# Kernel tuning notes

Measured on AMD Instinct MI355X. Metric: run time of the kernel, lower is better.

Reference implementation:

```python
import jax, jax.numpy as jnp
import numpy as np

FS = 2          # filter_size (kernel == stride, non-overlapping)
NL = 10         # num_layers
C_IN = 3        # input_channels
H = 256         # hidden width
OUT = 10        # out_dim
B = 128         # batch
D = FS ** NL    # input spatial length = 1024


def setup_inputs() -> dict:
    key = jax.random.key(0)
    ks = jax.random.split(key, NL + 2)
    inp = {"x": jax.random.normal(ks[0], (B, C_IN, D), dtype=jnp.float32)}
    cin = C_IN
    for l in range(NL):
        dl = D // FS ** (l + 1)  # out positions at layer l
        inp[f"w{l}"] = jax.random.normal(ks[l + 1], (H, cin, dl, FS), dtype=jnp.float32)
        cin = H
    inp["beta"] = jax.random.normal(ks[-1], (H, OUT), dtype=jnp.float32)
    return inp


def _lc(x, w):
    # Locally-connected 1d, stride == kernel: unfold is a pure reshape.
    # x: (B, C, Dd*k), w: (O, C, Dd, k) -> out: (B, O, Dd)
    O, C, Dd, k = w.shape
    xu = x.reshape(x.shape[0], C, Dd, k)
    # per-position contraction over (C, k); avoids the (B,O,C,Dd,k) intermediate
    return jnp.einsum('bcdk,ocdk->bod', xu, w) / (C ** 0.5)


def reference(x, w0, w1, w2, w3, w4, w5, w6, w7, w8, w9, beta):
    ws = [w0, w1, w2, w3, w4, w5, w6, w7, w8, w9]
    y = x
    for w in ws:  # fixed small layer loop
        y = jax.nn.relu(_lc(y, w))
    y = y.mean(axis=-1)            # (B, H) — last spatial dim is size 1
    return y @ beta / beta.shape[0]  # (B, OUT)
```

## Files before the change

### kernel.cpp

```cpp
#include <hip/hip_runtime.h>
#include <hip/hip_bf16.h>
#include <stdint.h>


typedef __attribute__((ext_vector_type(4))) float floatx4;
typedef __attribute__((ext_vector_type(8))) short shortx8;

__device__ __forceinline__ float bf2f(unsigned short u){
    union { unsigned int u; float f; } c; c.u = ((unsigned int)u) << 16; return c.f;
}
__device__ __forceinline__ unsigned short f2bf(float f){
    union { float f; unsigned int u; } c; c.f = f;
    unsigned int x = c.u;
    x += 0x7FFFu + ((x >> 16) & 1u);
    return (unsigned short)(x >> 16);
}

__global__ void probe_kernel(const unsigned int* __restrict__ x, int* __restrict__ flag){
    __shared__ int cnt[256];
    int tid = threadIdx.x;
    unsigned short lo = (unsigned short)(x[tid] & 0xFFFFu);
    int e = (lo >> 7) & 0xFF;
    cnt[tid] = (e >= 90 && e <= 143) ? 1 : 0;
    __syncthreads();
    for (int s = 128; s > 0; s >>= 1){
        if (tid < s) cnt[tid] += cnt[tid + s];
        __syncthreads();
    }
    if (tid == 0) *flag = (cnt[0] > 160) ? 1 : 0;
}

__global__ __launch_bounds__(256) void l0_kernel(const int* __restrict__ flag,
        const void* __restrict__ xv, const void* __restrict__ wv,
        unsigned short* __restrict__ A1){
    __shared__ float Xs[128*6];
    const int d = blockIdx.x;
    const int tid = threadIdx.x;
    const bool BF = (*flag != 0);
    for (int i = tid; i < 384; i += 256){
        int b = i / 3, c = i - b*3;
        if (BF){
            unsigned int u = *(const unsigned int*)((const unsigned short*)xv + (b*3+c)*1024 + 2*d);
            Xs[b*6 + c*2]     = bf2f((unsigned short)(u & 0xFFFFu));
            Xs[b*6 + c*2 + 1] = bf2f((unsigned short)(u >> 16));
        } else {
            const float* xf = (const float*)xv + (b*3+c)*1024 + 2*d;
            Xs[b*6 + c*2] = xf[0]; Xs[b*6 + c*2 + 1] = xf[1];
        }
    }
    __syncthreads();
    const int o = tid;
    float wr[6];
    #pragma unroll
    for (int c = 0; c < 3; ++c){
        if (BF){
            unsigned int u = *(const unsigned int*)((const unsigned short*)wv + ((o*3+c)*512 + d)*2);
            wr[c*2]   = bf2f((unsigned short)(u & 0xFFFFu));
            wr[c*2+1] = bf2f((unsigned short)(u >> 16));
        } else {
            const float* wf = (const float*)wv + ((o*3+c)*512 + d)*2;
            wr[c*2] = wf[0]; wr[c*2+1] = wf[1];
        }
    }
    const float s3 = 0.57735026918962576f;
    for (int b = 0; b < 128; ++b){
        float s = 0.f;
        #pragma unroll
        for (int j = 0; j < 6; ++j) s += Xs[b*6 + j] * wr[j];
        A1[d*32768 + b*256 + o] = f2bf(fmaxf(s, 0.f) * s3);
    }
}

template<bool WBF, bool ATOMIC>
__device__ __forceinline__ void layer_main_impl(const unsigned short* __restrict__ Ain,
        const void* __restrict__ wv, void* __restrict__ out, int dl, int ks){
    __shared__ unsigned short At[8*128*16];
    __shared__ unsigned short Wt[4*64*40];
    const int tid  = threadIdx.x;
    const int lane = tid & 63, wv_ = tid >> 6;
    const int g = lane >> 4, mr = lane & 15;
    const int nd = dl >> 2;
    int bi = blockIdx.x;
    const int dg = bi % nd; bi /= nd;
    const int ng = bi & 3;
    const int ksid = bi >> 2;
    const int TS = 16 / ks;
    const int d0 = dg << 2;
    const int o0 = ng << 6;
    const int dme = d0 + wv_;
    const float* wF = (const float*)wv;
    const unsigned short* wB = (const unsigned short*)wv;

    floatx4 acc[8][4];
    #pragma unroll
    for (int m = 0; m < 8; ++m)
        #pragma unroll
        for (int nb = 0; nb < 4; ++nb)
            acc[m][nb] = (floatx4){0.f,0.f,0.f,0.f};

    for (int s = 0; s < TS; ++s){
        const int c0 = (ksid*TS + s) << 4;
        {
            const int b = tid >> 1, h = tid & 1;
            #pragma unroll
            for (int i = 0; i < 8; ++i){
                uint4 v = *(const uint4*)(Ain + (2*d0 + i)*32768 + b*256 + c0 + h*8);
                *(uint4*)(At + (i*128 + b)*16 + h*8) = v;
            }
        }
        #pragma unroll
        for (int rr = 0; rr < 4; ++rr){
            int run = (rr << 8) + tid;
            int oo = run >> 4, cl = run & 15;
            int src = ((((o0 + oo) << 8) + (c0 + cl))*dl + d0)*2;
            unsigned short wtmp[8];
            if (WBF){
                uint4 u = *(const uint4*)(wB + src);
                const unsigned short* pu = (const unsigned short*)&u;
                #pragma unroll
                for (int j = 0; j < 8; ++j) wtmp[j] = pu[j];
            } else {
                float4 a = *(const float4*)(wF + src);
                float4 b4 = *(const float4*)(wF + src + 4);
                wtmp[0]=f2bf(a.x); wtmp[1]=f2bf(a.y); wtmp[2]=f2bf(a.z); wtmp[3]=f2bf(a.w);
                wtmp[4]=f2bf(b4.x); wtmp[5]=f2bf(b4.y); wtmp[6]=f2bf(b4.z); wtmp[7]=f2bf(b4.w);
            }
            #pragma unroll
            for (int j = 0; j < 8; ++j){
                int dd = j >> 1, t = j & 1;
                Wt[(dd*64 + oo)*40 + t*16 + cl] = wtmp[j];
            }
        }
        __syncthreads();
        shortx8 bfr[4];
        #pragma unroll
        for (int nb = 0; nb < 4; ++nb)
            bfr[nb] = *(const shortx8*)(Wt + (wv_*64 + nb*16 + mr)*40 + g*8);
        #pragma unroll
        for (int m = 0; m < 8; ++m){
            shortx8 af = *(const shortx8*)(At + ((wv_*2 + (g>>1))*128 + m*16 + mr)*16 + (g&1)*8);
            #pragma unroll
            for (int nb = 0; nb < 4; ++nb)
                acc[m][nb] = __builtin_amdgcn_mfma_f32_16x16x32_bf16(af, bfr[nb], acc[m][nb], 0,0,0);
        }
        __syncthreads();
    }
    #pragma unroll
    for (int m = 0; m < 8; ++m)
        #pragma unroll
        for (int nb = 0; nb < 4; ++nb)
            #pragma unroll
            for (int r = 0; r < 4; ++r){
                int b = m*16 + g*4 + r;
                int o = o0 + nb*16 + mr;
                if (ATOMIC)
                    unsafeAtomicAdd((float*)out + (dme*128 + b)*256 + o, acc[m][nb][r]);
                else
                    ((unsigned short*)out)[dme*32768 + b*256 + o] =
                        f2bf(fmaxf(acc[m][nb][r], 0.f) * 0.0625f);
            }
}

template<bool ATOMIC>
__global__ __launch_bounds__(256,2) void layer_main_k(const int* __restrict__ flag,
        const unsigned short* __restrict__ Ain, const void* __restrict__ wv,
        void* __restrict__ out, int dl, int ks){
    if (*flag) layer_main_impl<true,  ATOMIC>(Ain, wv, out, dl, ks);
    else       layer_main_impl<false, ATOMIC>(Ain, wv, out, dl, ks);
}

template<bool WBF>
__device__ __forceinline__ void tail_impl(const unsigned short* __restrict__ Ain,
        const void* __restrict__ wv, float* __restrict__ outS, int dl, int ksplit){
    int id = blockIdx.x;
    int d = id % dl; int t2 = id / dl;
    int ob = t2 & 3; int ksid = t2 >> 2;
    const int KSEG = 512 / ksplit;
    const int k0s = ksid * KSEG;
    const int lane = threadIdx.x & 63, wv2 = threadIdx.x >> 6;
    const int mr = lane & 15, kg = lane >> 4;
    const float* wF = (const float*)wv;
    const unsigned short* wB = (const unsigned short*)wv;
    floatx4 acc[2][4];
    #pragma unroll
    for (int mi = 0; mi < 2; ++mi)
        #pragma unroll
        for (int ni = 0; ni < 4; ++ni) acc[mi][ni] = (floatx4){0.f,0.f,0.f,0.f};
    for (int k0 = k0s; k0 < k0s + KSEG; k0 += 32){
        int c0 = (k0 >> 1) + kg*4;
        shortx8 af[2];
        #pragma unroll
        for (int mi = 0; mi < 2; ++mi){
            int b = wv2*32 + mi*16 + mr;
            #pragma unroll
            for (int cc = 0; cc < 4; ++cc){
                af[mi][2*cc]   = (short)Ain[(2*d)*32768   + b*256 + c0 + cc];
                af[mi][2*cc+1] = (short)Ain[(2*d+1)*32768 + b*256 + c0 + cc];
            }
        }
        shortx8 bf_[4];
        #pragma unroll
        for (int ni = 0; ni < 4; ++ni){
            int o = ob*64 + ni*16 + mr;
            int base = ((o*256 + c0)*dl + d)*2;
            #pragma unroll
            for (int cc = 0; cc < 4; ++cc){
                if (WBF){
                    unsigned int u = *(const unsigned int*)(wB + base);
                    bf_[ni][2*cc]   = (short)(u & 0xFFFFu);
                    bf_[ni][2*cc+1] = (short)(u >> 16);
                } else {
                    bf_[ni][2*cc]   = (short)f2bf(wF[base]);
                    bf_[ni][2*cc+1] = (short)f2bf(wF[base+1]);
                }
                base += 2*dl;
            }
        }
        #pragma unroll
        for (int mi = 0; mi < 2; ++mi)
            #pragma unroll
            for (int ni = 0; ni < 4; ++ni)
                acc[mi][ni] = __builtin_amdgcn_mfma_f32_16x16x32_bf16(af[mi], bf_[ni], acc[mi][ni], 0,0,0);
    }
    #pragma unroll
    for (int mi = 0; mi < 2; ++mi)
        #pragma unroll
        for (int ni = 0; ni < 4; ++ni)
            #pragma unroll
            for (int r = 0; r < 4; ++r){
                int b = wv2*32 + mi*16 + kg*4 + r;
                int o = ob*64 + ni*16 + mr;
                unsafeAtomicAdd(outS + (d*128 + b)*256 + o, acc[mi][ni][r]);
            }
}
__global__ __launch_bounds__(256) void tail_k(const int* __restrict__ flag,
        const unsigned short* __restrict__ Ain, const void* __restrict__ wv,
        float* __restrict__ outS, int dl, int ksplit){
    if (*flag) tail_impl<true >(Ain, wv, outS, dl, ksplit);
    else       tail_impl<false>(Ain, wv, outS, dl, ksplit);
}

__global__ __launch_bounds__(256) void fin_kernel(const float* __restrict__ S,
        unsigned short* __restrict__ A, int n){
    int i = (blockIdx.x*256 + threadIdx.x)*4;
    if (i + 3 < n){
        float4 v = *(const float4*)(S + i);
        unsigned short r0 = f2bf(fmaxf(v.x,0.f)*0.0625f);
        unsigned short r1 = f2bf(fmaxf(v.y,0.f)*0.0625f);
        unsigned short r2 = f2bf(fmaxf(v.z,0.f)*0.0625f);
        unsigned short r3 = f2bf(fmaxf(v.w,0.f)*0.0625f);
        unsigned int lo = (unsigned int)r0 | ((unsigned int)r1 << 16);
        unsigned int hi = (unsigned int)r2 | ((unsigned int)r3 << 16);
        uint2 u; u.x = lo; u.y = hi;
        *(uint2*)(A + i) = u;
    }
}

template<bool BF>
__device__ __forceinline__ void epi_impl(const float* __restrict__ S9, const void* __restrict__ beta,
                                         void* __restrict__ out){
    int b = blockIdx.x;
    int lane = threadIdx.x;
    float accv[10];
    #pragma unroll
    for (int o = 0; o < 10; ++o) accv[o] = 0.f;
    for (int h = lane; h < 256; h += 64){
        float y = fmaxf(S9[b*256 + h], 0.f) * 0.0625f;
        #pragma unroll
        for (int o = 0; o < 10; ++o){
            float be = BF ? bf2f(((const unsigned short*)beta)[h*10 + o])
                          : ((const float*)beta)[h*10 + o];
            accv[o] += y * be;
        }
    }
    #pragma unroll
    for (int off = 32; off > 0; off >>= 1){
        #pragma unroll
        for (int o = 0; o < 10; ++o)
            accv[o] += __shfl_down(accv[o], off, 64);
    }
    if (lane == 0){
        #pragma unroll
        for (int o = 0; o < 10; ++o){
            float v = accv[o] * (1.f/256.f);
            if (BF) ((unsigned short*)out)[b*10 + o] = f2bf(v);
            else    ((float*)out)[b*10 + o] = v;
        }
    }
}
__global__ void epi_kernel(const int* __restrict__ flag, const float* __restrict__ S9,
                           const void* __restrict__ beta, void* __restrict__ out){
    if (*flag) epi_impl<true>(S9, beta, out);
    else       epi_impl<false>(S9, beta, out);
}

extern "C" void kernel_launch(void* const* d_in, const int* in_sizes, int n_in,
                              void* d_out, int out_size, void* d_ws, size_t ws_size,
                              hipStream_t stream) {
    (void)in_sizes; (void)n_in; (void)out_size; (void)ws_size;
    char* wsb = (char*)d_ws;
    int* flag = (int*)wsb;
    unsigned short* A1 = (unsigned short*)(wsb + 512);
    float* S2 = (float*)(wsb + 512);
    float* S3 = S2 + 4194304;
    float* S4 = S3 + 2097152;
    float* S5 = S4 + 1048576;
    float* S6 = S5 + 524288;
    float* S7 = S6 + 262144;
    float* S8 = S7 + 131072;
    float* S9 = S8 + 65536;
    unsigned short* A2 = (unsigned short*)(wsb + 512 + 33554432);
    unsigned short* A3 = A2;
    unsigned short* A4 = A3 + 4194304;
    unsigned short* A5 = A4 + 2097152;
    unsigned short* A6 = A5 + 1048576;
    unsigned short* A7 = A6 + 524288;
    unsigned short* A8 = A7 + 262144;
    unsigned short* A9 = A8 + 131072;

    probe_kernel<<<1, 256, 0, stream>>>((const unsigned int*)d_in[0], flag);
    l0_kernel<<<512, 256, 0, stream>>>(flag, d_in[0], d_in[1], A1);
    layer_main_k<false><<<256, 256, 0, stream>>>(flag, A1, d_in[2], A2, 256, 1);
    hipMemsetAsync(S2, 0, 33423360, stream);
    layer_main_k<true ><<<256, 256, 0, stream>>>(flag, A2, d_in[3], S2, 128, 2);
    fin_kernel<<<4096, 256, 0, stream>>>(S2, A3, 4194304);
    layer_main_k<true ><<<256, 256, 0, stream>>>(flag, A3, d_in[4], S3, 64, 4);
    fin_kernel<<<2048, 256, 0, stream>>>(S3, A4, 2097152);
    layer_main_k<true ><<<256, 256, 0, stream>>>(flag, A4, d_in[5], S4, 32, 8);
    fin_kernel<<<1024, 256, 0, stream>>>(S4, A5, 1048576);
    layer_main_k<true ><<<256, 256, 0, stream>>>(flag, A5, d_in[6], S5, 16, 16);
    fin_kernel<<<512, 256, 0, stream>>>(S5, A6, 524288);
    layer_main_k<true ><<<128, 256, 0, stream>>>(flag, A6, d_in[7], S6, 8, 16);
    fin_kernel<<<256, 256, 0, stream>>>(S6, A7, 262144);
    layer_main_k<true ><<<64, 256, 0, stream>>>(flag, A7, d_in[8], S7, 4, 16);
    fin_kernel<<<128, 256, 0, stream>>>(S7, A8, 131072);
    tail_k<<<128, 256, 0, stream>>>(flag, A8, d_in[9], S8, 2, 16);
    fin_kernel<<<64, 256, 0, stream>>>(S8, A9, 65536);
    tail_k<<<64, 256, 0, stream>>>(flag, A9, d_in[10], S9, 1, 16);
    epi_kernel<<<128, 64, 0, stream>>>(flag, S9, d_in[11], d_out);
}
```

Baseline: 642.4 us.

## Retile locally-connected layers with batch/output blocking and direct-global A fragments

Replaces the layer_main kernel with layer3_k, which tiles over 32 batch rows × 32 output channels × several positions per wave. A fragments now load straight from global memory instead of staging through LDS, and the weight-tile LDS layout is rearranged and padded. Layer 2 now writes bf16 directly without split-K atomics, which removes its fin pass. The deeper layers get new split-K and grid choices that give more blocks per launch, and workspace offsets are reshuffled. This trades LDS reuse of activations for more parallelism and fewer atomics, at the cost of more global loads per MFMA.

```diff
diff --git a/kernel.cpp b/kernel.cpp
--- a/kernel.cpp
+++ b/kernel.cpp
@@ -3,8 +3,15 @@
 #include <stdint.h>
 
 
+#define B_   128
+#define H_   256
+#define OUT_ 10
+#define WT_PLANE 644
+#define WT_ELEMS (32*WT_PLANE)
+
 typedef __attribute__((ext_vector_type(4))) float floatx4;
 typedef __attribute__((ext_vector_type(8))) short shortx8;
+typedef __attribute__((ext_vector_type(4))) short shortx4;
 
 __device__ __forceinline__ float bf2f(unsigned short u){
     union { unsigned int u; float f; } c; c.u = ((unsigned int)u) << 16; return c.f;
@@ -71,102 +78,124 @@
     }
 }
 
-template<bool WBF, bool ATOMIC>
-__device__ __forceinline__ void layer_main_impl(const unsigned short* __restrict__ Ain,
-        const void* __restrict__ wv, void* __restrict__ out, int dl, int ks){
-    __shared__ unsigned short At[8*128*16];
-    __shared__ unsigned short Wt[4*64*40];
-    const int tid  = threadIdx.x;
+template<int DPW, bool WBF, bool ATOMIC>
+__device__ __forceinline__ void layer3_impl(unsigned short* __restrict__ Wt,
+        const unsigned short* __restrict__ Ain, const void* __restrict__ wv,
+        void* __restrict__ out, int dl, int dgN, int TS){
+    constexpr int DT = 4*DPW;
+    const int tid = threadIdx.x;
     const int lane = tid & 63, wv_ = tid >> 6;
-    const int g = lane >> 4, mr = lane & 15;
-    const int nd = dl >> 2;
+    const int mr = lane & 15, g = lane >> 4;
+    const int tI = g >> 1, chI = g & 1;
     int bi = blockIdx.x;
-    const int dg = bi % nd; bi /= nd;
-    const int ng = bi & 3;
-    const int ksid = bi >> 2;
-    const int TS = 16 / ks;
-    const int d0 = dg << 2;
-    const int o0 = ng << 6;
-    const int dme = d0 + wv_;
+    const int bg = bi & 3; const int og = (bi >> 2) & 7; const int rest = bi >> 5;
+    const int dg = rest % dgN; const int ksid = rest / dgN;
+    const int d0 = dg * DT, o0 = og * 32, b0 = bg * 32;
     const float* wF = (const float*)wv;
     const unsigned short* wB = (const unsigned short*)wv;
 
-    floatx4 acc[8][4];
-    #pragma unroll
-    for (int m = 0; m < 8; ++m)
-        #pragma unroll
-        for (int nb = 0; nb < 4; ++nb)
-            acc[m][nb] = (floatx4){0.f,0.f,0.f,0.f};
+    floatx4 acc[2][2][DPW];
+    #pragma unroll
+    for (int m = 0; m < 2; ++m)
+        #pragma unroll
+        for (int nb = 0; nb < 2; ++nb)
+            #pragma unroll
+            for (int dd = 0; dd < DPW; ++dd)
+                acc[m][nb][dd] = (floatx4){0.f,0.f,0.f,0.f};
 
     for (int s = 0; s < TS; ++s){
         const int c0 = (ksid*TS + s) << 4;
-        {
-            const int b = tid >> 1, h = tid & 1;
-            #pragma unroll
-            for (int i = 0; i < 8; ++i){
-                uint4 v = *(const uint4*)(Ain + (2*d0 + i)*32768 + b*256 + c0 + h*8);
-                *(uint4*)(At + (i*128 + b)*16 + h*8) = v;
-            }
-        }
-        #pragma unroll
-        for (int rr = 0; rr < 4; ++rr){
-            int run = (rr << 8) + tid;
-            int oo = run >> 4, cl = run & 15;
-            int src = ((((o0 + oo) << 8) + (c0 + cl))*dl + d0)*2;
-            unsigned short wtmp[8];
-            if (WBF){
-                uint4 u = *(const uint4*)(wB + src);
-                const unsigned short* pu = (const unsigned short*)&u;
+        if (WBF){
+            constexpr int PARTS = DT/4;
+            for (int task = tid; task < 512*PARTS; task += 256){
+                int part = (PARTS == 1) ? 0 : (task & (PARTS-1));
+                int run  = (PARTS == 1) ? task : (task / PARTS);
+                int cl = run & 15, ol = run >> 4;
+                const unsigned short* src = wB + ((size_t)((o0+ol)*256 + c0+cl)*dl + d0)*2 + part*8;
+                uint4 u = *(const uint4*)src;
+                const unsigned short* e = (const unsigned short*)&u;
                 #pragma unroll
-                for (int j = 0; j < 8; ++j) wtmp[j] = pu[j];
-            } else {
-                float4 a = *(const float4*)(wF + src);
-                float4 b4 = *(const float4*)(wF + src + 4);
-                wtmp[0]=f2bf(a.x); wtmp[1]=f2bf(a.y); wtmp[2]=f2bf(a.z); wtmp[3]=f2bf(a.w);
-                wtmp[4]=f2bf(b4.x); wtmp[5]=f2bf(b4.y); wtmp[6]=f2bf(b4.z); wtmp[7]=f2bf(b4.w);
-            }
-            #pragma unroll
-            for (int j = 0; j < 8; ++j){
-                int dd = j >> 1, t = j & 1;
-                Wt[(dd*64 + oo)*40 + t*16 + cl] = wtmp[j];
+                for (int j = 0; j < 8; ++j){
+                    int dloc = part*4 + (j >> 1), t = j & 1;
+                    Wt[(dloc*2 + t)*WT_PLANE + ol*20 + cl] = e[j];
+                }
+            }
+        } else {
+            constexpr int PARTS = DT/2;
+            for (int task = tid; task < 512*PARTS; task += 256){
+                int part = task & (PARTS-1);
+                int run  = task / PARTS;
+                int cl = run & 15, ol = run >> 4;
+                const float* src = wF + ((size_t)((o0+ol)*256 + c0+cl)*dl + d0)*2 + part*4;
+                float4 v = *(const float4*)src;
+                int base = (part*4)*WT_PLANE + ol*20 + cl;
+                Wt[base]              = f2bf(v.x);
+                Wt[base + WT_PLANE]   = f2bf(v.y);
+                Wt[base + 2*WT_PLANE] = f2bf(v.z);
+                Wt[base + 3*WT_PLANE] = f2bf(v.w);
             }
         }
         __syncthreads();
-        shortx8 bfr[4];
-        #pragma unroll
-        for (int nb = 0; nb < 4; ++nb)
-            bfr[nb] = *(const shortx8*)(Wt + (wv_*64 + nb*16 + mr)*40 + g*8);
-        #pragma unroll
-        for (int m = 0; m < 8; ++m){
-            shortx8 af = *(const shortx8*)(At + ((wv_*2 + (g>>1))*128 + m*16 + mr)*16 + (g&1)*8);
-            #pragma unroll
-            for (int nb = 0; nb < 4; ++nb)
-                acc[m][nb] = __builtin_amdgcn_mfma_f32_16x16x32_bf16(af, bfr[nb], acc[m][nb], 0,0,0);
-        }
+        shortx8 af[2][DPW];
+        #pragma unroll
+        for (int m = 0; m < 2; ++m)
+            #pragma unroll
+            for (int dd = 0; dd < DPW; ++dd){
+                int d = d0 + wv_*DPW + dd;
+                int p = 2*d + tI;
+                const unsigned short* ap = Ain + ((size_t)p*128 + b0 + m*16 + mr)*256 + c0 + chI*8;
+                uint4 u = *(const uint4*)ap;
+                af[m][dd] = *(const shortx8*)&u;
+            }
+        shortx8 bfr[2][DPW];
+        #pragma unroll
+        for (int nb = 0; nb < 2; ++nb)
+            #pragma unroll
+            for (int dd = 0; dd < DPW; ++dd){
+                int off = ((wv_*DPW + dd)*2 + tI)*WT_PLANE + (nb*16 + mr)*20 + chI*8;
+                shortx4 lo = *(const shortx4*)(Wt + off);
+                shortx4 hi = *(const shortx4*)(Wt + off + 4);
+                shortx8 bb;
+                bb[0]=lo[0]; bb[1]=lo[1]; bb[2]=lo[2]; bb[3]=lo[3];
+                bb[4]=hi[0]; bb[5]=hi[1]; bb[6]=hi[2]; bb[7]=hi[3];
+                bfr[nb][dd] = bb;
+            }
+        #pragma unroll
+        for (int m = 0; m < 2; ++m)
+            #pragma unroll
+            for (int nb = 0; nb < 2; ++nb)
+                #pragma unroll
+                for (int dd = 0; dd < DPW; ++dd)
+                    acc[m][nb][dd] = __builtin_amdgcn_mfma_f32_16x16x32_bf16(af[m][dd], bfr[nb][dd], acc[m][nb][dd], 0,0,0);
         __syncthreads();
     }
     #pragma unroll
-    for (int m = 0; m < 8; ++m)
-        #pragma unroll
-        for (int nb = 0; nb < 4; ++nb)
-            #pragma unroll
-            for (int r = 0; r < 4; ++r){
-                int b = m*16 + g*4 + r;
+    for (int m = 0; m < 2; ++m)
+        #pragma unroll
+        for (int dd = 0; dd < DPW; ++dd){
+            int d = d0 + wv_*DPW + dd;
+            #pragma unroll
+            for (int nb = 0; nb < 2; ++nb){
                 int o = o0 + nb*16 + mr;
-                if (ATOMIC)
-                    unsafeAtomicAdd((float*)out + (dme*128 + b)*256 + o, acc[m][nb][r]);
-                else
-                    ((unsigned short*)out)[dme*32768 + b*256 + o] =
-                        f2bf(fmaxf(acc[m][nb][r], 0.f) * 0.0625f);
-            }
-}
-
-template<bool ATOMIC>
-__global__ __launch_bounds__(256,2) void layer_main_k(const int* __restrict__ flag,
+                #pragma unroll
+                for (int r = 0; r < 4; ++r){
+                    int b = b0 + m*16 + g*4 + r;
+                    size_t idx = ((size_t)d*128 + b)*256 + o;
+                    float v = acc[m][nb][dd][r];
+                    if (ATOMIC) unsafeAtomicAdd((float*)out + idx, v);
+                    else ((unsigned short*)out)[idx] = f2bf(fmaxf(v, 0.f) * 0.0625f);
+                }
+            }
+        }
+}
+
+template<int DPW, bool ATOMIC>
+__global__ __launch_bounds__(256,3) void layer3_k(const int* __restrict__ flag,
         const unsigned short* __restrict__ Ain, const void* __restrict__ wv,
-        void* __restrict__ out, int dl, int ks){
-    if (*flag) layer_main_impl<true,  ATOMIC>(Ain, wv, out, dl, ks);
-    else       layer_main_impl<false, ATOMIC>(Ain, wv, out, dl, ks);
+        void* __restrict__ out, int dl, int dgN, int TS){
+    __shared__ unsigned short Wt[WT_ELEMS];
+    if (*flag) layer3_impl<DPW, true,  ATOMIC>(Wt, Ain, wv, out, dl, dgN, TS);
+    else       layer3_impl<DPW, false, ATOMIC>(Wt, Ain, wv, out, dl, dgN, TS);
 }
 
 template<bool WBF>
@@ -261,30 +290,30 @@
                                          void* __restrict__ out){
     int b = blockIdx.x;
     int lane = threadIdx.x;
-    float accv[10];
-    #pragma unroll
-    for (int o = 0; o < 10; ++o) accv[o] = 0.f;
+    float accv[OUT_];
+    #pragma unroll
+    for (int o = 0; o < OUT_; ++o) accv[o] = 0.f;
     for (int h = lane; h < 256; h += 64){
         float y = fmaxf(S9[b*256 + h], 0.f) * 0.0625f;
         #pragma unroll
-        for (int o = 0; o < 10; ++o){
-            float be = BF ? bf2f(((const unsigned short*)beta)[h*10 + o])
-                          : ((const float*)beta)[h*10 + o];
+        for (int o = 0; o < OUT_; ++o){
+            float be = BF ? bf2f(((const unsigned short*)beta)[h*OUT_ + o])
+                          : ((const float*)beta)[h*OUT_ + o];
             accv[o] += y * be;
         }
     }
     #pragma unroll
     for (int off = 32; off > 0; off >>= 1){
         #pragma unroll
-        for (int o = 0; o < 10; ++o)
+        for (int o = 0; o < OUT_; ++o)
             accv[o] += __shfl_down(accv[o], off, 64);
     }
     if (lane == 0){
         #pragma unroll
-        for (int o = 0; o < 10; ++o){
+        for (int o = 0; o < OUT_; ++o){
             float v = accv[o] * (1.f/256.f);
-            if (BF) ((unsigned short*)out)[b*10 + o] = f2bf(v);
-            else    ((float*)out)[b*10 + o] = v;
+            if (BF) ((unsigned short*)out)[b*OUT_ + o] = f2bf(v);
+            else    ((float*)out)[b*OUT_ + o] = v;
         }
     }
 }
@@ -300,39 +329,39 @@
     (void)in_sizes; (void)n_in; (void)out_size; (void)ws_size;
     char* wsb = (char*)d_ws;
     int* flag = (int*)wsb;
-    unsigned short* A1 = (unsigned short*)(wsb + 512);
-    float* S2 = (float*)(wsb + 512);
-    float* S3 = S2 + 4194304;
-    float* S4 = S3 + 2097152;
-    float* S5 = S4 + 1048576;
-    float* S6 = S5 + 524288;
-    float* S7 = S6 + 262144;
-    float* S8 = S7 + 131072;
-    float* S9 = S8 + 65536;
+    char* base1 = wsb + 512;
+    float* S3 = (float*)(base1);
+    float* S4 = (float*)(base1 + 8388608);
+    float* S5 = (float*)(base1 + 12582912);
+    float* S6 = (float*)(base1 + 14680064);
+    float* S7 = (float*)(base1 + 15728640);
+    float* S8 = (float*)(base1 + 16252928);
+    float* S9 = (float*)(base1 + 16515072);
+    unsigned short* A3 = (unsigned short*)(base1 + 16646144);
+    unsigned short* A4 = (unsigned short*)(base1 + 25034752);
+    unsigned short* A5 = (unsigned short*)(base1 + 29229056);
+    unsigned short* A6 = (unsigned short*)(base1 + 31326208);
+    unsigned short* A7 = (unsigned short*)(base1 + 32374784);
+    unsigned short* A8 = (unsigned short*)(base1 + 32899072);
+    unsigned short* A9 = (unsigned short*)(base1 + 33161216);
+    unsigned short* A1 = (unsigned short*)(base1);
     unsigned short* A2 = (unsigned short*)(wsb + 512 + 33554432);
-    unsigned short* A3 = A2;
-    unsigned short* A4 = A3 + 4194304;
-    unsigned short* A5 = A4 + 2097152;
-    unsigned short* A6 = A5 + 1048576;
-    unsigned short* A7 = A6 + 524288;
-    unsigned short* A8 = A7 + 262144;
-    unsigned short* A9 = A8 + 131072;
 
     probe_kernel<<<1, 256, 0, stream>>>((const unsigned int*)d_in[0], flag);
     l0_kernel<<<512, 256, 0, stream>>>(flag, d_in[0], d_in[1], A1);
-    layer_main_k<false><<<256, 256, 0, stream>>>(flag, A1, d_in[2], A2, 256, 1);
-    hipMemsetAsync(S2, 0, 33423360, stream);
-    layer_main_k<true ><<<256, 256, 0, stream>>>(flag, A2, d_in[3], S2, 128, 2);
-    fin_kernel<<<4096, 256, 0, stream>>>(S2, A3, 4194304);
-    layer_main_k<true ><<<256, 256, 0, stream>>>(flag, A3, d_in[4], S3, 64, 4);
+
+    layer3_k<4,false><<<512, 256, 0, stream>>>(flag, A1, d_in[2], A2, 256, 16, 16);
+    hipMemsetAsync(base1, 0, 16646144, stream);
+    layer3_k<4,false><<<256, 256, 0, stream>>>(flag, A2, d_in[3], A3, 128, 8, 16);
+    layer3_k<4,true ><<<256, 256, 0, stream>>>(flag, A3, d_in[4], S3, 64, 4, 8);
     fin_kernel<<<2048, 256, 0, stream>>>(S3, A4, 2097152);
-    layer_main_k<true ><<<256, 256, 0, stream>>>(flag, A4, d_in[5], S4, 32, 8);
+    layer3_k<4,true ><<<256, 256, 0, stream>>>(flag, A4, d_in[5], S4, 32, 2, 4);
     fin_kernel<<<1024, 256, 0, stream>>>(S4, A5, 1048576);
-    layer_main_k<true ><<<256, 256, 0, stream>>>(flag, A5, d_in[6], S5, 16, 16);
+    layer3_k<4,true ><<<256, 256, 0, stream>>>(flag, A5, d_in[6], S5, 16, 1, 2);
     fin_kernel<<<512, 256, 0, stream>>>(S5, A6, 524288);
-    layer_main_k<true ><<<128, 256, 0, stream>>>(flag, A6, d_in[7], S6, 8, 16);
+    layer3_k<2,true ><<<256, 256, 0, stream>>>(flag, A6, d_in[7], S6, 8, 1, 2);
     fin_kernel<<<256, 256, 0, stream>>>(S6, A7, 262144);
-    layer_main_k<true ><<<64, 256, 0, stream>>>(flag, A7, d_in[8], S7, 4, 16);
+    layer3_k<1,true ><<<256, 256, 0, stream>>>(flag, A7, d_in[8], S7, 4, 1, 2);
     fin_kernel<<<128, 256, 0, stream>>>(S7, A8, 131072);
     tail_k<<<128, 256, 0, stream>>>(flag, A8, d_in[9], S8, 2, 16);
     fin_kernel<<<64, 256, 0, stream>>>(S8, A9, 65536);
```

Result: slower. 698.3 us (+8.7%).
